# Kernel tuning notes

Measured on AMD Instinct MI355X. Metric: run time of the kernel, lower is better.

## Reference

```python
import jax, jax.numpy as jnp
import numpy as np

N_NODES = 50000
N_EDGES = 800000
NFEAT, NHID, NCLASS = 512, 64, 40


def setup_inputs() -> dict:
    key = jax.random.key(0)
    ks = jax.random.split(key, 10)
    x = jax.random.normal(ks[0], (N_NODES, NFEAT), dtype=jnp.float32)
    edge_weight = jax.random.uniform(ks[1], (N_EDGES,), dtype=jnp.float32)
    W1 = jax.random.normal(ks[2], (NFEAT, NHID), dtype=jnp.float32) / np.sqrt(NFEAT)
    b1 = jnp.zeros((NHID,), dtype=jnp.float32)
    W2 = jax.random.normal(ks[3], (NHID, NHID), dtype=jnp.float32) / np.sqrt(NHID)
    b2 = jnp.zeros((NHID,), dtype=jnp.float32)
    W3 = jax.random.normal(ks[4], (NHID, NCLASS), dtype=jnp.float32) / np.sqrt(NHID)
    b3 = jnp.zeros((NCLASS,), dtype=jnp.float32)
    row = jax.random.randint(ks[5], (N_EDGES,), 0, N_NODES, dtype=jnp.int32)
    col = jax.random.randint(ks[6], (N_EDGES,), 0, N_NODES, dtype=jnp.int32)
    return {"x": x, "edge_weight": edge_weight, "W1": W1, "b1": b1,
            "W2": W2, "b2": b2, "W3": W3, "b3": b3, "row": row, "col": col}


def _gcn_layer(h, W, b, row, col, ew):
    # support = h @ W + b ; out = spmm(adj, support)
    support = h @ W + b                      # [N, dout]
    msg = support[col] * ew[:, None]         # gather + scale, [E, dout]
    return jax.ops.segment_sum(msg, row, num_segments=N_NODES)


def reference(x, edge_weight, W1, b1, W2, b2, W3, b3, row, col):
    h = jax.nn.relu(_gcn_layer(x, W1, b1, row, col, edge_weight))
    # dropout: eval mode -> identity
    h = _gcn_layer(h, W2, b2, row, col, edge_weight)
    h = _gcn_layer(h, W3, b3, row, col, edge_weight)
    return jax.nn.log_softmax(h, axis=1)
```

## Files before the change

### kernel.cpp

```cpp
#include <hip/hip_runtime.h>
#include <hip/hip_bf16.h>

#define NNODES 50000
#define NEDGES 800000
#define NFEAT  512
#define NHID   64
#define NCLASS 40

#define CAP 48
#define CNTSTRIDE 16
#define EPT 4
#define FILL_CHUNKS ((NEDGES / EPT + 255) / 256)
#define GEMM1_BLOCKS ((NNODES + 31) / 32)
#define SPMM_BLOCKS ((NNODES + 15) / 16)

typedef __attribute__((ext_vector_type(8))) short short8;
typedef __attribute__((ext_vector_type(4))) float floatx4;

static __device__ __forceinline__ unsigned short f2bf(float f) {
    union { float f; unsigned u; } v; v.f = f;
    const unsigned r = v.u + 0x7fffu + ((v.u >> 16) & 1u);
    return (unsigned short)(r >> 16);
}
static __device__ __forceinline__ float bf2f(unsigned u) {
    union { unsigned u; float f; } v; v.u = u << 16;
    return v.f;
}

template<int NCB, int NVALID>
static __device__ __forceinline__ void convW_body(
    const float* __restrict__ W, unsigned short* __restrict__ wb, int idx) {
    const int lane = idx & 63;
    const int cb   = (idx >> 6) % NCB;
    const int kb   = idx / (64 * NCB);
    const int q = lane >> 4, m = lane & 15;
    const int c = cb * 16 + m;
    short8 v;
    #pragma unroll
    for (int j = 0; j < 8; ++j)
        v[j] = (c < NVALID)
             ? (short)f2bf(W[(size_t)(kb * 32 + q * 8 + j) * NVALID + c])
             : (short)0;
    *(short8*)(wb + (size_t)idx * 8) = v;
}

__global__ __launch_bounds__(256) void conv_kernel(
    const float* __restrict__ W1, unsigned short* __restrict__ wb1,
    const float* __restrict__ W2, unsigned short* __restrict__ wb2,
    const float* __restrict__ W3, unsigned short* __restrict__ wb3,
    int4* __restrict__ cnt4) {
    const int blk = blockIdx.x;
    const int tid = threadIdx.x;
    if (blk < 16) {
        convW_body<4, 64>(W1, wb1, blk * 256 + tid);
    } else if (blk < 18) {
        convW_body<4, 64>(W2, wb2, (blk - 16) * 256 + tid);
    } else if (blk < 20) {
        const int idx = (blk - 18) * 256 + tid;
        if (idx < 2 * 3 * 64) convW_body<3, 40>(W3, wb3, idx);
    } else {
        const int i = (blk - 20) * 256 + tid;
        if (i < NNODES * CNTSTRIDE / 4) cnt4[i] = make_int4(0, 0, 0, 0);
    }
}

__global__ __launch_bounds__(256) void bucket_gemm1_kernel(
    const int* __restrict__ row, const int* __restrict__ col,
    const float* __restrict__ ew, int* __restrict__ cnt,
    unsigned* __restrict__ bucket,
    const float* __restrict__ x, const unsigned short* __restrict__ wb,
    const float* __restrict__ b, unsigned short* __restrict__ outb) {
    const int blk  = blockIdx.x;
    const int tid  = threadIdx.x;
    const int base = blk / 3;
    const int r    = blk % 3;

    if (r == 2) {
        const int e = (base * 256 + tid) * EPT;
        if (e >= NEDGES) return;
        const int4   r4 = *(const int4*)(row + e);
        const int4   c4 = *(const int4*)(col + e);
        const float4 w4 = *(const float4*)(ew + e);
        const int p0 = atomicAdd(&cnt[r4.x * CNTSTRIDE], 1);
        const int p1 = atomicAdd(&cnt[r4.y * CNTSTRIDE], 1);
        const int p2 = atomicAdd(&cnt[r4.z * CNTSTRIDE], 1);
        const int p3 = atomicAdd(&cnt[r4.w * CNTSTRIDE], 1);
        if (p0 < CAP) bucket[(size_t)r4.x * CAP + p0] = (unsigned)c4.x | ((unsigned)f2bf(w4.x) << 16);
        if (p1 < CAP) bucket[(size_t)r4.y * CAP + p1] = (unsigned)c4.y | ((unsigned)f2bf(w4.y) << 16);
        if (p2 < CAP) bucket[(size_t)r4.z * CAP + p2] = (unsigned)c4.z | ((unsigned)f2bf(w4.z) << 16);
        if (p3 < CAP) bucket[(size_t)r4.w * CAP + p3] = (unsigned)c4.w | ((unsigned)f2bf(w4.w) << 16);
        return;
    }

    const int g = base * 2 + r;
    if (g >= GEMM1_BLOCKS) return;
    __shared__ float red[2][16][64];

    const int lane = tid & 63;
    const int wid  = tid >> 6;
    const int p  = wid >> 1;
    const int kh = wid & 1;
    const int q = lane >> 4, m = lane & 15;

    const int rowbase = g * 32 + p * 16;
    int rload = rowbase + m;
    if (rload >= NNODES) rload = NNODES - 1;
    const float* xp = x + (size_t)rload * NFEAT + kh * 256 + q * 8;

    floatx4 acc[4];
    #pragma unroll
    for (int cb = 0; cb < 4; ++cb) acc[cb] = (floatx4)0.f;

    #pragma unroll
    for (int kc = 0; kc < 2; ++kc) {
        float4 a0[4], a1[4];
        #pragma unroll
        for (int u = 0; u < 4; ++u) {
            a0[u] = *(const float4*)(xp + (kc * 4 + u) * 32);
            a1[u] = *(const float4*)(xp + (kc * 4 + u) * 32 + 4);
        }
        #pragma unroll
        for (int u = 0; u < 4; ++u) {
            short8 afrag;
            afrag[0] = (short)f2bf(a0[u].x); afrag[1] = (short)f2bf(a0[u].y);
            afrag[2] = (short)f2bf(a0[u].z); afrag[3] = (short)f2bf(a0[u].w);
            afrag[4] = (short)f2bf(a1[u].x); afrag[5] = (short)f2bf(a1[u].y);
            afrag[6] = (short)f2bf(a1[u].z); afrag[7] = (short)f2bf(a1[u].w);

            const int kbg = kh * 8 + kc * 4 + u;
            const unsigned short* wp = wb + ((size_t)(kbg * 4) * 64 + lane) * 8;
            #pragma unroll
            for (int cb = 0; cb < 4; ++cb) {
                const short8 bfrag = *(const short8*)(wp + (size_t)cb * 64 * 8);
                acc[cb] = __builtin_amdgcn_mfma_f32_16x16x32_bf16(
                    afrag, bfrag, acc[cb], 0, 0, 0);
            }
        }
    }

    if (kh == 1) {
        #pragma unroll
        for (int cb = 0; cb < 4; ++cb)
            #pragma unroll
            for (int i = 0; i < 4; ++i)
                red[p][q * 4 + i][cb * 16 + m] = acc[cb][i];
    }
    __syncthreads();
    if (kh == 1) return;

    const int orow = rowbase + q * 4;
    #pragma unroll
    for (int cb = 0; cb < 4; ++cb) {
        const int c = cb * 16 + m;
        const float bias = b[c];
        #pragma unroll
        for (int i = 0; i < 4; ++i) {
            const int rr2 = orow + i;
            if (rr2 < NNODES)
                outb[(size_t)rr2 * NHID + c] =
                    f2bf(acc[cb][i] + red[p][q * 4 + i][c] + bias);
        }
    }
}

template<bool RELU, int NCB, int NOUT>
__global__ __launch_bounds__(256) void spmm_gemm_kernel(
    const unsigned short* __restrict__ supb, const unsigned* __restrict__ bucket,
    const int* __restrict__ cnt, const unsigned short* __restrict__ wb,
    const float* __restrict__ bias, unsigned short* __restrict__ outb) {
    __shared__ unsigned ent[16][CAP];
    __shared__ unsigned short ht[16 * 72];

    const int tid  = threadIdx.x;
    const int wid  = tid >> 6;
    const int lane = tid & 63;
    const int half = lane >> 5;
    const int fp   = lane & 31;
    const int nb0  = blockIdx.x * 16;

    #pragma unroll
    for (int s = 0; s < 3; ++s) {
        const int idx = s * 256 + tid;
        const int ln  = idx / CAP;
        const int sl  = idx - ln * CAP;
        const int n   = nb0 + ln;
        int d = cnt[n * CNTSTRIDE];
        if (d > CAP) d = CAP;
        ent[ln][sl] = (sl < d) ? bucket[(size_t)n * CAP + sl] : 0u;
    }
    __syncthreads();

    const int lnb = wid * 4;
    float a0[4] = {0.f, 0.f, 0.f, 0.f}, a1[4] = {0.f, 0.f, 0.f, 0.f};
    int maxd = 0;
    #pragma unroll
    for (int jn = 0; jn < 4; ++jn) {
        int d = cnt[(nb0 + lnb + jn) * CNTSTRIDE];
        if (d > CAP) d = CAP;
        maxd = max(maxd, d);
    }

    for (int i = half; i < maxd; i += 8) {
        unsigned eb[4][4], vb[4][4];
        #pragma unroll
        for (int jn = 0; jn < 4; ++jn)
            #pragma unroll
            for (int j = 0; j < 4; ++j)
                eb[jn][j] = ent[lnb + jn][i + 2 * j];
        #pragma unroll
        for (int jn = 0; jn < 4; ++jn)
            #pragma unroll
            for (int j = 0; j < 4; ++j)
                vb[jn][j] = *(const unsigned*)(supb + (size_t)(eb[jn][j] & 0xffffu) * NHID + fp * 2);
        #pragma unroll
        for (int jn = 0; jn < 4; ++jn)
            #pragma unroll
            for (int j = 0; j < 4; ++j) {
                const float w = bf2f(eb[jn][j] >> 16);
                a0[jn] += w * bf2f(vb[jn][j] & 0xffffu);
                a1[jn] += w * bf2f(vb[jn][j] >> 16);
            }
    }
    #pragma unroll
    for (int jn = 0; jn < 4; ++jn) {
        a0[jn] += __shfl_xor(a0[jn], 32);
        a1[jn] += __shfl_xor(a1[jn], 32);
        if (RELU) { a0[jn] = fmaxf(a0[jn], 0.f); a1[jn] = fmaxf(a1[jn], 0.f); }
    }
    if (half == 0) {
        #pragma unroll
        for (int jn = 0; jn < 4; ++jn)
            *(unsigned*)&ht[(lnb + jn) * 72 + fp * 2] =
                (unsigned)f2bf(a0[jn]) | ((unsigned)f2bf(a1[jn]) << 16);
    }
    __syncthreads();

    if (wid != 0) return;
    const int q = lane >> 4, m = lane & 15;
    const unsigned short* hp = &ht[m * 72 + q * 8];

    floatx4 acc[NCB];
    #pragma unroll
    for (int cb = 0; cb < NCB; ++cb) acc[cb] = (floatx4)0.f;

    #pragma unroll
    for (int kb = 0; kb < 2; ++kb) {
        const short8 afrag = *(const short8*)(hp + kb * 32);
        const unsigned short* wp = wb + ((size_t)(kb * NCB) * 64 + lane) * 8;
        #pragma unroll
        for (int cb = 0; cb < NCB; ++cb) {
            const short8 bfrag = *(const short8*)(wp + (size_t)cb * 64 * 8);
            acc[cb] = __builtin_amdgcn_mfma_f32_16x16x32_bf16(
                afrag, bfrag, acc[cb], 0, 0, 0);
        }
    }

    const int rbase = nb0 + q * 4;
    #pragma unroll
    for (int cb = 0; cb < NCB; ++cb) {
        const int c = cb * 16 + m;
        if (c >= NOUT) continue;
        const float bv = bias[c];
        #pragma unroll
        for (int i = 0; i < 4; ++i)
            outb[(size_t)(rbase + i) * NOUT + c] = f2bf(acc[cb][i] + bv);
    }
}

__global__ __launch_bounds__(256) void spmm_bf40_lsm_kernel(
    const unsigned short* __restrict__ supb, const unsigned* __restrict__ bucket,
    const int* __restrict__ cnt, float* __restrict__ out) {
    __shared__ unsigned ent[4][CAP];

    const int tid = threadIdx.x;
    const int f   = tid & 63;
    const int wid = tid >> 6;
    const int nb0 = blockIdx.x * 4;

    if (tid < 4 * CAP) {
        const int ln = tid / CAP;
        const int sl = tid - ln * CAP;
        int d = cnt[(nb0 + ln) * CNTSTRIDE];
        if (d > CAP) d = CAP;
        ent[ln][sl] = (sl < d) ? bucket[(size_t)(nb0 + ln) * CAP + sl] : 0u;
    }
    __syncthreads();

    const int n = nb0 + wid;
    int deg = cnt[n * CNTSTRIDE];
    if (deg > CAP) deg = CAP;
    float acc = 0.f;
    if (f < NCLASS) {
        for (int i = 0; i < deg; i += 16) {
            unsigned eb[16]; float vb[16];
            #pragma unroll
            for (int j = 0; j < 16; ++j)
                eb[j] = ent[wid][min(i + j, CAP - 1)];
            #pragma unroll
            for (int j = 0; j < 16; ++j)
                vb[j] = bf2f(supb[(size_t)(eb[j] & 0xffffu) * NCLASS + f]);
            #pragma unroll
            for (int j = 0; j < 16; ++j)
                acc += vb[j] * bf2f(eb[j] >> 16);
        }
    }
    float m = (f < NCLASS) ? acc : -1e30f;
    #pragma unroll
    for (int o = 32; o > 0; o >>= 1) m = fmaxf(m, __shfl_xor(m, o));
    float ex = (f < NCLASS) ? __expf(acc - m) : 0.f;
    #pragma unroll
    for (int o = 32; o > 0; o >>= 1) ex += __shfl_xor(ex, o);
    const float ls = __logf(ex) + m;
    if (f < NCLASS) out[(size_t)n * NCLASS + f] = acc - ls;
}

extern "C" void kernel_launch(void* const* d_in, const int* in_sizes, int n_in,
                              void* d_out, int out_size, void* d_ws, size_t ws_size,
                              hipStream_t stream) {
    const float* x  = (const float*)d_in[0];
    const float* ew = (const float*)d_in[1];
    const float* W1 = (const float*)d_in[2];
    const float* b1 = (const float*)d_in[3];
    const float* W2 = (const float*)d_in[4];
    const float* b2 = (const float*)d_in[5];
    const float* W3 = (const float*)d_in[6];
    const float* b3 = (const float*)d_in[7];
    const int* row  = (const int*)d_in[8];
    const int* col  = (const int*)d_in[9];
    float* out = (float*)d_out;

    const size_t n64 = (size_t)NNODES * NHID;
    const size_t n40 = (size_t)NNODES * NCLASS;
    unsigned* bucket = (unsigned*)d_ws;
    int* cnt = (int*)(bucket + (size_t)NNODES * CAP);
    unsigned short* S1 = (unsigned short*)(cnt + (size_t)NNODES * CNTSTRIDE);
    unsigned short* S2 = S1 + n64;
    unsigned short* S3 = S2 + n64;
    unsigned short* wb1 = S3 + n40;
    unsigned short* wb2 = wb1 + 16 * 4 * 64 * 8;
    unsigned short* wb3 = wb2 + 2 * 4 * 64 * 8;

    conv_kernel<<<820, 256, 0, stream>>>(W1, wb1, W2, wb2, W3, wb3, (int4*)cnt);

    bucket_gemm1_kernel<<<3 * FILL_CHUNKS, 256, 0, stream>>>(
        row, col, ew, cnt, bucket, x, wb1, b1, S1);

    spmm_gemm_kernel<true, 4, 64><<<SPMM_BLOCKS, 256, 0, stream>>>(
        S1, bucket, cnt, wb2, b2, S2);

    spmm_gemm_kernel<false, 3, 40><<<SPMM_BLOCKS, 256, 0, stream>>>(
        S2, bucket, cnt, wb3, b3, S3);

    spmm_bf40_lsm_kernel<<<(NNODES + 3) / 4, 256, 0, stream>>>(S3, bucket, cnt, out);
}
```

Before: 268.7 us.

## Fuse last two SpMM layers and log-softmax into one cooperative persistent kernel

```diff
diff --git a/kernel.cpp b/kernel.cpp
--- a/kernel.cpp
+++ b/kernel.cpp
@@ -1,5 +1,8 @@
 #include <hip/hip_runtime.h>
 #include <hip/hip_bf16.h>
+#include <hip/hip_cooperative_groups.h>
+
+namespace cg = cooperative_groups;
 
 #define NNODES 50000
 #define NEDGES 800000
@@ -13,6 +16,7 @@
 #define FILL_CHUNKS ((NEDGES / EPT + 255) / 256)
 #define GEMM1_BLOCKS ((NNODES + 31) / 32)
 #define SPMM_BLOCKS ((NNODES + 15) / 16)
+#define LSM_BLOCKS ((NNODES + 3) / 4)
 
 typedef __attribute__((ext_vector_type(8))) short short8;
 typedef __attribute__((ext_vector_type(4))) float floatx4;
@@ -164,19 +168,18 @@
 }
 
 template<bool RELU, int NCB, int NOUT>
-__global__ __launch_bounds__(256) void spmm_gemm_kernel(
-    const unsigned short* __restrict__ supb, const unsigned* __restrict__ bucket,
-    const int* __restrict__ cnt, const unsigned short* __restrict__ wb,
-    const float* __restrict__ bias, unsigned short* __restrict__ outb) {
-    __shared__ unsigned ent[16][CAP];
-    __shared__ unsigned short ht[16 * 72];
-
+static __device__ __forceinline__ void spmm_layer_body(
+    int blk, const unsigned short* __restrict__ supb,
+    const unsigned* __restrict__ bucket, const int* __restrict__ cnt,
+    const unsigned short* __restrict__ wb, const float* __restrict__ bias,
+    unsigned short* __restrict__ outb,
+    unsigned (*ent)[CAP], unsigned short* ht) {
     const int tid  = threadIdx.x;
     const int wid  = tid >> 6;
     const int lane = tid & 63;
     const int half = lane >> 5;
     const int fp   = lane & 31;
-    const int nb0  = blockIdx.x * 16;
+    const int nb0  = blk * 16;
 
     #pragma unroll
     for (int s = 0; s < 3; ++s) {
@@ -235,47 +238,49 @@
     }
     __syncthreads();
 
-    if (wid != 0) return;
-    const int q = lane >> 4, m = lane & 15;
-    const unsigned short* hp = &ht[m * 72 + q * 8];
-
-    floatx4 acc[NCB];
-    #pragma unroll
-    for (int cb = 0; cb < NCB; ++cb) acc[cb] = (floatx4)0.f;
-
-    #pragma unroll
-    for (int kb = 0; kb < 2; ++kb) {
-        const short8 afrag = *(const short8*)(hp + kb * 32);
-        const unsigned short* wp = wb + ((size_t)(kb * NCB) * 64 + lane) * 8;
+    if (wid == 0) {
+        const int q = lane >> 4, m = lane & 15;
+        const unsigned short* hp = &ht[m * 72 + q * 8];
+
+        floatx4 acc[NCB];
+        #pragma unroll
+        for (int cb = 0; cb < NCB; ++cb) acc[cb] = (floatx4)0.f;
+
+        #pragma unroll
+        for (int kb = 0; kb < 2; ++kb) {
+            const short8 afrag = *(const short8*)(hp + kb * 32);
+            const unsigned short* wp = wb + ((size_t)(kb * NCB) * 64 + lane) * 8;
+            #pragma unroll
+            for (int cb = 0; cb < NCB; ++cb) {
+                const short8 bfrag = *(const short8*)(wp + (size_t)cb * 64 * 8);
+                acc[cb] = __builtin_amdgcn_mfma_f32_16x16x32_bf16(
+                    afrag, bfrag, acc[cb], 0, 0, 0);
+            }
+        }
+
+        const int rbase = nb0 + q * 4;
         #pragma unroll
         for (int cb = 0; cb < NCB; ++cb) {
-            const short8 bfrag = *(const short8*)(wp + (size_t)cb * 64 * 8);
-            acc[cb] = __builtin_amdgcn_mfma_f32_16x16x32_bf16(
-                afrag, bfrag, acc[cb], 0, 0, 0);
-        }
-    }
-
-    const int rbase = nb0 + q * 4;
-    #pragma unroll
-    for (int cb = 0; cb < NCB; ++cb) {
-        const int c = cb * 16 + m;
-        if (c >= NOUT) continue;
-        const float bv = bias[c];
-        #pragma unroll
-        for (int i = 0; i < 4; ++i)
-            outb[(size_t)(rbase + i) * NOUT + c] = f2bf(acc[cb][i] + bv);
-    }
-}
-
-__global__ __launch_bounds__(256) void spmm_bf40_lsm_kernel(
-    const unsigned short* __restrict__ supb, const unsigned* __restrict__ bucket,
-    const int* __restrict__ cnt, float* __restrict__ out) {
-    __shared__ unsigned ent[4][CAP];
-
+            const int c = cb * 16 + m;
+            if (c < NOUT) {
+                const float bv = bias[c];
+                #pragma unroll
+                for (int i = 0; i < 4; ++i)
+                    outb[(size_t)(rbase + i) * NOUT + c] = f2bf(acc[cb][i] + bv);
+            }
+        }
+    }
+    __syncthreads();
+}
+
+static __device__ __forceinline__ void lsm_body(
+    int blk, const unsigned short* __restrict__ supb,
+    const unsigned* __restrict__ bucket, const int* __restrict__ cnt,
+    float* __restrict__ out, unsigned (*ent)[CAP]) {
     const int tid = threadIdx.x;
     const int f   = tid & 63;
     const int wid = tid >> 6;
-    const int nb0 = blockIdx.x * 4;
+    const int nb0 = blk * 4;
 
     if (tid < 4 * CAP) {
         const int ln = tid / CAP;
@@ -312,6 +317,45 @@
     for (int o = 32; o > 0; o >>= 1) ex += __shfl_xor(ex, o);
     const float ls = __logf(ex) + m;
     if (f < NCLASS) out[(size_t)n * NCLASS + f] = acc - ls;
+    __syncthreads();
+}
+
+__global__ __launch_bounds__(256) void spmm3_kernel(
+    const unsigned short* __restrict__ S1, const unsigned* __restrict__ bucket,
+    const int* __restrict__ cnt,
+    const unsigned short* __restrict__ wb2, const float* __restrict__ b2,
+    unsigned short* __restrict__ S2,
+    const unsigned short* __restrict__ wb3, const float* __restrict__ b3,
+    unsigned short* __restrict__ S3, float* __restrict__ out) {
+    __shared__ unsigned ent[16][CAP];
+    __shared__ unsigned short ht[16 * 72];
+    cg::grid_group grid = cg::this_grid();
+
+    for (int g = blockIdx.x; g < SPMM_BLOCKS; g += gridDim.x)
+        spmm_layer_body<true, 4, 64>(g, S1, bucket, cnt, wb2, b2, S2, ent, ht);
+    grid.sync();
+    for (int g = blockIdx.x; g < SPMM_BLOCKS; g += gridDim.x)
+        spmm_layer_body<false, 3, 40>(g, S2, bucket, cnt, wb3, b3, S3, ent, ht);
+    grid.sync();
+    for (int g = blockIdx.x; g < LSM_BLOCKS; g += gridDim.x)
+        lsm_body(g, S3, bucket, cnt, out, ent);
+}
+
+template<bool RELU, int NCB, int NOUT>
+__global__ __launch_bounds__(256) void spmm_gemm_kernel(
+    const unsigned short* __restrict__ supb, const unsigned* __restrict__ bucket,
+    const int* __restrict__ cnt, const unsigned short* __restrict__ wb,
+    const float* __restrict__ bias, unsigned short* __restrict__ outb) {
+    __shared__ unsigned ent[16][CAP];
+    __shared__ unsigned short ht[16 * 72];
+    spmm_layer_body<RELU, NCB, NOUT>(blockIdx.x, supb, bucket, cnt, wb, bias, outb, ent, ht);
+}
+
+__global__ __launch_bounds__(256) void spmm_bf40_lsm_kernel(
+    const unsigned short* __restrict__ supb, const unsigned* __restrict__ bucket,
+    const int* __restrict__ cnt, float* __restrict__ out) {
+    __shared__ unsigned ent[16][CAP];
+    lsm_body(blockIdx.x, supb, bucket, cnt, out, ent);
 }
 
 extern "C" void kernel_launch(void* const* d_in, const int* in_sizes, int n_in,
@@ -345,11 +389,34 @@
     bucket_gemm1_kernel<<<3 * FILL_CHUNKS, 256, 0, stream>>>(
         row, col, ew, cnt, bucket, x, wb1, b1, S1);
 
-    spmm_gemm_kernel<true, 4, 64><<<SPMM_BLOCKS, 256, 0, stream>>>(
-        S1, bucket, cnt, wb2, b2, S2);
-
-    spmm_gemm_kernel<false, 3, 40><<<SPMM_BLOCKS, 256, 0, stream>>>(
-        S2, bucket, cnt, wb3, b3, S3);
-
-    spmm_bf40_lsm_kernel<<<(NNODES + 3) / 4, 256, 0, stream>>>(S3, bucket, cnt, out);
-}
+    static int coopGrid = -1;
+    if (coopGrid == -1) {
+        int maxBlk = 0;
+        hipError_t oe = hipOccupancyMaxActiveBlocksPerMultiprocessor(
+            &maxBlk, reinterpret_cast<const void*>(spmm3_kernel), 256, 0);
+        if (oe == hipSuccess && maxBlk > 0) {
+            long g = (long)maxBlk * 256;
+            coopGrid = (int)(g < SPMM_BLOCKS ? g : SPMM_BLOCKS);
+        } else {
+            coopGrid = 0;
+        }
+    }
+    bool done = false;
+    if (coopGrid > 0) {
+        void* args[] = {(void*)&S1, (void*)&bucket, (void*)&cnt,
+                        (void*)&wb2, (void*)&b2, (void*)&S2,
+                        (void*)&wb3, (void*)&b3, (void*)&S3, (void*)&out};
+        hipError_t err = hipLaunchCooperativeKernel(
+            reinterpret_cast<void*>(spmm3_kernel),
+            dim3(coopGrid), dim3(256), args, 0, stream);
+        if (err == hipSuccess) done = true;
+        else coopGrid = 0;
+    }
+    if (!done) {
+        spmm_gemm_kernel<true, 4, 64><<<SPMM_BLOCKS, 256, 0, stream>>>(
+            S1, bucket, cnt, wb2, b2, S2);
+        spmm_gemm_kernel<false, 3, 40><<<SPMM_BLOCKS, 256, 0, stream>>>(
+            S2, bucket, cnt, wb3, b3, S3);
+        spmm_bf40_lsm_kernel<<<LSM_BLOCKS, 256, 0, stream>>>(S3, bucket, cnt, out);
+    }
+}
```

New measurement: 490.6 us. 1.83x slower.
